# Performance work log

Hardware: AMD Instinct MI355X
Metric: run time of the kernel (lower is better)

## Reference

```python
import jax, jax.numpy as jnp
import numpy as np

T, B, D = 1024, 8, 1024
H, DH, FF = 16, 64, 4096
BG = 0.1  # GRU gating bias constant
SCALE = 1.0 / DH ** 0.5


def layer_norm(x, g, b, eps=1e-5):
    mu = jnp.mean(x, axis=-1, keepdims=True)
    var = jnp.var(x, axis=-1, keepdims=True)
    return (x - mu) * jax.lax.rsqrt(var + eps) * g + b


def gru_gate(x, y, W, U, bz):
    # W, U: [3, D, D] stacking (r, z, g) projections; bz: Uz bias
    r = jax.nn.sigmoid(y @ W[0] + x @ U[0])
    z = jax.nn.sigmoid(y @ W[1] + x @ U[1] + bz - BG)
    h = jnp.tanh(y @ W[2] + r * (x @ U[2]))
    return (1.0 - z) * x + z * h


def setup_inputs() -> dict:
    key = jax.random.key(0)
    ks = jax.random.split(key, 16)
    s = 0.02
    inp = {
        "x": jax.random.normal(ks[0], (T, B, D), jnp.float32),
        "Wq": jax.random.normal(ks[1], (D, H * DH), jnp.float32) * s,
        "Wk": jax.random.normal(ks[2], (D, H * DH), jnp.float32) * s,
        "Wv": jax.random.normal(ks[3], (D, H * DH), jnp.float32) * s,
        "Wo": jax.random.normal(ks[4], (H * DH, D), jnp.float32) * s,
        "ln1_g": jnp.ones((D,), jnp.float32),
        "ln1_b": jnp.zeros((D,), jnp.float32),
        "W1": jax.random.normal(ks[5], (D, FF), jnp.float32) * s,
        "b1": jnp.zeros((FF,), jnp.float32),
        "W2": jax.random.normal(ks[6], (FF, D), jnp.float32) * s,
        "b2": jnp.zeros((D,), jnp.float32),
        "ln2_g": jnp.ones((D,), jnp.float32),
        "ln2_b": jnp.zeros((D,), jnp.float32),
        "gate1_W": jax.random.normal(ks[7], (3, D, D), jnp.float32) * s,
        "gate1_U": jax.random.normal(ks[8], (3, D, D), jnp.float32) * s,
        "gate1_bz": jnp.zeros((D,), jnp.float32),
        "gate2_W": jax.random.normal(ks[9], (3, D, D), jnp.float32) * s,
        "gate2_U": jax.random.normal(ks[10], (3, D, D), jnp.float32) * s,
        "gate2_bz": jnp.zeros((D,), jnp.float32),
        "attn_mask": jnp.triu(jnp.ones((T, T), bool), k=1),  # causal: mask j > i
    }
    return inp


def reference(x, Wq, Wk, Wv, Wo, ln1_g, ln1_b, W1, b1, W2, b2,
              ln2_g, ln2_b, gate1_W, gate1_U, gate1_bz,
              gate2_W, gate2_U, gate2_bz, attn_mask):
    # --- multihead attention (pre_lnorm=True) ---
    xn = layer_norm(x, ln1_g, ln1_b)                     # [T,B,D]
    q = (xn @ Wq).reshape(T, B, H, DH)
    k = (xn @ Wk).reshape(T, B, H, DH)
    v = (xn @ Wv).reshape(T, B, H, DH)
    scores = jnp.einsum('ibhd,jbhd->ijbh', q, k) * SCALE  # [T,T,B,H]
    scores = jnp.where(attn_mask[:, :, None, None], -jnp.inf, scores)
    probs = jax.nn.softmax(scores, axis=1)
    attn = jnp.einsum('ijbh,jbhd->ibhd', probs, v).reshape(T, B, H * DH)
    src2 = attn @ Wo                                      # [T,B,D]
    # --- GRU gate 1 ---
    src = gru_gate(x, src2, gate1_W, gate1_U, gate1_bz)
    # --- positionwise FFN (pre_lnorm=True) ---
    sn = layer_norm(src, ln2_g, ln2_b)
    ff = jax.nn.relu(sn @ W1 + b1) @ W2 + b2
    # --- GRU gate 2 ---
    return gru_gate(src, ff, gate2_W, gate2_U, gate2_bz)
```

## Files before the change

kernel.cpp:

```cpp
#include <hip/hip_runtime.h>
#include <hip/hip_bf16.h>

#define T_  1024
#define B_  8
#define D_  1024
#define H_  16
#define DH_ 64
#define FF_ 4096
#define MROWS (T_*B_)

typedef __attribute__((ext_vector_type(8))) short short8;
typedef __attribute__((ext_vector_type(4))) float f32x4;
typedef __attribute__((ext_vector_type(4))) unsigned short us4;
typedef __attribute__((ext_vector_type(4))) unsigned int  u32x4;

__device__ __forceinline__ unsigned short f2b(float f){
  unsigned int u = __builtin_bit_cast(unsigned int, f);
  u += 0x7FFFu + ((u >> 16) & 1u);
  return (unsigned short)(u >> 16);
}
__device__ __forceinline__ float b2f(unsigned short h){
  unsigned int u = ((unsigned int)h) << 16;
  return __builtin_bit_cast(float, u);
}

__device__ __forceinline__ void glds16(const unsigned short* g, unsigned short* l){
  __builtin_amdgcn_global_load_lds(
    (const __attribute__((address_space(1))) unsigned int*)g,
    (__attribute__((address_space(3))) unsigned int*)l, 16, 0, 0);
}

enum { FRELU=1 };

__global__ __launch_bounds__(512, 2) void gemm256(
    const unsigned short* __restrict__ A1, const unsigned short* __restrict__ A2,
    int K1, long lda,
    const unsigned short* __restrict__ Bt, long ldb,
    unsigned short* __restrict__ C, long ldc,
    const float* __restrict__ bias, int K, int flags)
{
  constexpr int BM = 256, BK = 32;
  extern __shared__ char L[];

  int t = threadIdx.x, w = t >> 6, l = t & 63;

  int nx = gridDim.x;
  int nwg = nx * gridDim.y;
  int lin = blockIdx.y*nx + blockIdx.x;
  if (!(nwg & 7)) lin = (lin & 7)*(nwg >> 3) + (lin >> 3);
  int bx = lin % nx, by = lin / nx;
  int m0 = by*BM, n0 = bx*BM;

  int srow[2], sce[2];
  #pragma unroll
  for (int q=0;q<2;q++){
    int p  = q*8192 + w*1024 + l*16;
    int sp = p ^ (((p>>6)&3)<<4);
    srow[q] = sp >> 6;
    sce[q]  = (sp & 63) >> 1;
  }

  auto stage = [&](int buf, int kt){
    int k0 = kt*BK;
    const unsigned short* ap; int ko;
    if (k0 < K1){ ap = A1; ko = k0; } else { ap = A2; ko = k0 - K1; }
    char* ab = L + buf*32768;
    char* bb = ab + 16384;
    #pragma unroll
    for (int q=0;q<2;q++)
      glds16(ap + (long)(m0 + srow[q])*lda + ko + sce[q],
             (unsigned short*)(ab + q*8192 + w*1024));
    #pragma unroll
    for (int q=0;q<2;q++)
      glds16(Bt + (long)(n0 + srow[q])*ldb + k0 + sce[q],
             (unsigned short*)(bb + q*8192 + w*1024));
  };

  f32x4 acc[8][4];
  #pragma unroll
  for (int m=0;m<8;m++)
    #pragma unroll
    for (int n=0;n<4;n++) acc[m][n] = (f32x4){0.f,0.f,0.f,0.f};

  int wr = w >> 2, wc = w & 3;
  int fr = l & 15, fq = l >> 4;
  int nk = K / BK;

  stage(0, 0);
  stage(1, 1);
  asm volatile("s_waitcnt vmcnt(4)" ::: "memory");
  __builtin_amdgcn_s_barrier();
  asm volatile("" ::: "memory");

  int cur = 0;
  for (int kt = 0; kt < nk; ++kt){
    int nxt = cur + 2; if (nxt >= 3) nxt -= 3;
    if (kt + 2 < nk) stage(nxt, kt + 2);

    const char* ab = L + cur*32768;
    const char* bb = ab + 16384;
    short8 af[8], bf[4];
    #pragma unroll
    for (int n=0;n<4;n++){
      int r = wc*64 + n*16 + fr;
      bf[n] = *(const short8*)(bb + ((r*64 + fq*16) ^ ((r&3)<<4)));
    }
    #pragma unroll
    for (int m=0;m<8;m++){
      int r = wr*128 + m*16 + fr;
      af[m] = *(const short8*)(ab + ((r*64 + fq*16) ^ ((r&3)<<4)));
    }
    __builtin_amdgcn_s_setprio(1);
    #pragma unroll
    for (int m=0;m<8;m++)
      #pragma unroll
      for (int n=0;n<4;n++)
        acc[m][n] = __builtin_amdgcn_mfma_f32_16x16x32_bf16(af[m], bf[n], acc[m][n], 0,0,0);
    __builtin_amdgcn_s_setprio(0);

    if (kt + 2 < nk) asm volatile("s_waitcnt vmcnt(4)" ::: "memory");
    else             asm volatile("s_waitcnt vmcnt(0)" ::: "memory");
    __builtin_amdgcn_s_barrier();
    asm volatile("" ::: "memory");
    cur += 1; if (cur >= 3) cur -= 3;
  }

  int r0 = m0 + wr*128 + (fq << 2);
  int c0 = n0 + wc*64 + fr;
  #pragma unroll
  for (int m=0;m<8;m++)
    #pragma unroll
    for (int n=0;n<4;n++){
      int col = c0 + n*16;
      float bv = bias ? bias[col] : 0.f;
      #pragma unroll
      for (int j=0;j<4;j++){
        float v = acc[m][n][j] + bv;
        if (flags & FRELU) v = v > 0.f ? v : 0.f;
        C[(long)(r0 + m*16 + j)*ldc + col] = f2b(v);
      }
    }
}

__global__ __launch_bounds__(256) void gemm_bf16(
    const unsigned short* __restrict__ A1, const unsigned short* __restrict__ A2,
    int K1, long lda,
    const unsigned short* __restrict__ Bt, long ldb,
    unsigned short* __restrict__ C, long ldc,
    const float* __restrict__ bias, int K, int flags)
{
  constexpr int BM = 128, BK = 32;
  __shared__ unsigned short As[2][BM*BK];
  __shared__ unsigned short Bs[2][BM*BK];

  int t = threadIdx.x, w = t >> 6, l = t & 63;

  int nx = gridDim.x;
  int nwg = nx * gridDim.y;
  int lin = blockIdx.y*nx + blockIdx.x;
  if (!(nwg & 7)) lin = (lin & 7)*(nwg >> 3) + (lin >> 3);
  int bx = lin % nx, by = lin / nx;
  int m0 = by*BM, n0 = bx*BM;

  int arow = t >> 2, acol = (t & 3) * 8;
  const unsigned short* a1p = A1 + (long)(m0 + arow)*lda + acol;
  const unsigned short* a2p = A2 + (long)(m0 + arow)*lda + acol - K1;
  const unsigned short* bp  = Bt + (long)(n0 + arow)*ldb + acol;

  auto stage = [&](int buf, int k0){
    const unsigned short* ap = (k0 < K1) ? a1p : a2p;
    glds16(ap + k0,          &As[buf][      w*512]);
    glds16(ap + 64*lda + k0, &As[buf][2048 + w*512]);
    glds16(bp + k0,          &Bs[buf][      w*512]);
    glds16(bp + 64*ldb + k0, &Bs[buf][2048 + w*512]);
  };

  f32x4 acc[4][4];
  #pragma unroll
  for (int m=0;m<4;m++)
    #pragma unroll
    for (int n=0;n<4;n++) acc[m][n] = (f32x4){0.f,0.f,0.f,0.f};

  int wm = (w >> 1) * 64, wn = (w & 1) * 64;
  int fr = l & 15, fk = (l >> 4) * 8;
  int nk = K / BK;

  stage(0, 0);
  __syncthreads();

  for (int kt = 0; kt < nk; ++kt){
    int cur = kt & 1;
    if (kt + 1 < nk) stage(cur ^ 1, (kt+1)*BK);

    short8 af[4], bf[4];
    #pragma unroll
    for (int m=0;m<4;m++) af[m] = *(const short8*)&As[cur][(wm + m*16 + fr)*BK + fk];
    #pragma unroll
    for (int n=0;n<4;n++) bf[n] = *(const short8*)&Bs[cur][(wn + n*16 + fr)*BK + fk];
    #pragma unroll
    for (int m=0;m<4;m++)
      #pragma unroll
      for (int n=0;n<4;n++)
        acc[m][n] = __builtin_amdgcn_mfma_f32_16x16x32_bf16(af[m], bf[n], acc[m][n], 0, 0, 0);

    __syncthreads();
  }

  int r0 = m0 + wm + ((l >> 4) << 2);
  int c0 = n0 + wn + fr;
  #pragma unroll
  for (int m=0;m<4;m++)
    #pragma unroll
    for (int n=0;n<4;n++){
      int col = c0 + n*16;
      float bv = bias ? bias[col] : 0.f;
      #pragma unroll
      for (int j=0;j<4;j++){
        float v = acc[m][n][j] + bv;
        if (flags & FRELU) v = v > 0.f ? v : 0.f;
        C[(long)(r0 + m*16 + j)*ldc + col] = f2b(v);
      }
    }
}

__global__ __launch_bounds__(256) void flash_attn(
  const unsigned short* __restrict__ qkv, const unsigned short* __restrict__ vT,
  unsigned short* __restrict__ O)
{
  int p = blockIdx.x, z = blockIdx.y;
  int b = z >> 4, h = z & 15;
  const unsigned short* Vz = vT + (long)z*DH_*T_;

  __shared__ unsigned short Ks[64*64];
  __shared__ unsigned short Vs[64*64];
  __shared__ unsigned short Ps[4][32][72];

  int t = threadIdx.x, w = t >> 6, l = t & 63;
  int fr = l & 15, fg = l >> 4;
  int srow = t >> 2, sc = (t & 3) * 16;

  for (int rep = 0; rep < 2; ++rep){
    int qt = rep ? (7 - p) : p;
    int q0 = qt*128 + w*32;

    short8 qf[2][2];
    #pragma unroll
    for (int m=0;m<2;m++)
      #pragma unroll
      for (int ks=0;ks<2;ks++)
        qf[m][ks] = *(const short8*)(qkv + ((long)(q0 + m*16 + fr)*B_ + b)*3072 + h*DH_ + ks*32 + fg*8);

    f32x4 oacc[2][4];
    float mr[2][4], lr[2][4];
    #pragma unroll
    for (int m=0;m<2;m++){
      #pragma unroll
      for (int n=0;n<4;n++) oacc[m][n] = (f32x4){0.f,0.f,0.f,0.f};
      #pragma unroll
      for (int j=0;j<4;j++){ mr[m][j] = -1e30f; lr[m][j] = 0.f; }
    }

    int nkv = (qt + 1) * 2;
    for (int kt = 0; kt < nkv; ++kt){
      int kv0 = kt * 64;
      __syncthreads();
      {
        const unsigned short* kg = qkv + ((long)(kv0+srow)*B_ + b)*3072 + 1024 + h*DH_ + sc;
        const unsigned short* vg = Vz + (long)srow*T_ + kv0 + sc;
        int rb = srow*128, sw = (srow & 7) << 4;
        *(u32x4*)((char*)Ks + ((rb + sc*2     ) ^ sw)) = *(const u32x4*)(kg);
        *(u32x4*)((char*)Ks + ((rb + sc*2 + 16) ^ sw)) = *(const u32x4*)(kg + 8);
        *(u32x4*)((char*)Vs + ((rb + sc*2     ) ^ sw)) = *(const u32x4*)(vg);
        *(u32x4*)((char*)Vs + ((rb + sc*2 + 16) ^ sw)) = *(const u32x4*)(vg + 8);
      }
      __syncthreads();

      if (kv0 <= q0 + 31){
        f32x4 sacc[2][4];
        #pragma unroll
        for (int m=0;m<2;m++)
          #pragma unroll
          for (int n=0;n<4;n++) sacc[m][n] = (f32x4){0.f,0.f,0.f,0.f};
        __builtin_amdgcn_s_setprio(1);
        #pragma unroll
        for (int ks=0;ks<2;ks++){
          short8 kf[4];
          #pragma unroll
          for (int n=0;n<4;n++){
            int r = n*16 + fr;
            kf[n] = *(const short8*)((const char*)Ks + ((r*128 + ks*64 + fg*16) ^ ((r & 7) << 4)));
          }
          #pragma unroll
          for (int m=0;m<2;m++)
            #pragma unroll
            for (int n=0;n<4;n++)
              sacc[m][n] = __builtin_amdgcn_mfma_f32_16x16x32_bf16(qf[m][ks], kf[n], sacc[m][n], 0,0,0);
        }
        __builtin_amdgcn_s_setprio(0);

        #pragma unroll
        for (int m=0;m<2;m++)
          #pragma unroll
          for (int j=0;j<4;j++){
            int qg = q0 + m*16 + fg*4 + j;
            float vmax = -1e30f;
            #pragma unroll
            for (int n=0;n<4;n++){
              int kg = kv0 + n*16 + fr;
              float s = (kg <= qg) ? sacc[m][n][j]*0.125f : -1e30f;
              sacc[m][n][j] = s;
              vmax = fmaxf(vmax, s);
            }
            #pragma unroll
            for (int msk=1; msk<16; msk<<=1) vmax = fmaxf(vmax, __shfl_xor(vmax, msk));
            float mnew = fmaxf(mr[m][j], vmax);
            float sc_o = __expf(mr[m][j] - mnew);
            mr[m][j] = mnew;
            float rsum = 0.f;
            #pragma unroll
            for (int n=0;n<4;n++){
              float pv = __expf(sacc[m][n][j] - mnew);
              sacc[m][n][j] = pv;
              rsum += pv;
            }
            #pragma unroll
            for (int msk=1; msk<16; msk<<=1) rsum += __shfl_xor(rsum, msk);
            lr[m][j] = lr[m][j]*sc_o + rsum;
            #pragma unroll
            for (int n=0;n<4;n++) oacc[m][n][j] *= sc_o;
          }

        #pragma unroll
        for (int m=0;m<2;m++)
          #pragma unroll
          for (int n=0;n<4;n++)
            #pragma unroll
            for (int j=0;j<4;j++)
              Ps[w][m*16 + fg*4 + j][n*16 + fr] = f2b(sacc[m][n][j]);

        __builtin_amdgcn_s_setprio(1);
        #pragma unroll
        for (int ks=0;ks<2;ks++){
          short8 pf[2], vf[4];
          #pragma unroll
          for (int m=0;m<2;m++) pf[m] = *(const short8*)&Ps[w][m*16+fr][ks*32+fg*8];
          #pragma unroll
          for (int n=0;n<4;n++){
            int r = n*16 + fr;
            vf[n] = *(const short8*)((const char*)Vs + ((r*128 + ks*64 + fg*16) ^ ((r & 7) << 4)));
          }
          #pragma unroll
          for (int m=0;m<2;m++)
            #pragma unroll
            for (int n=0;n<4;n++)
              oacc[m][n] = __builtin_amdgcn_mfma_f32_16x16x32_bf16(pf[m], vf[n], oacc[m][n], 0,0,0);
        }
        __builtin_amdgcn_s_setprio(0);
      }
    }

    #pragma unroll
    for (int m=0;m<2;m++)
      #pragma unroll
      for (int j=0;j<4;j++){
        float inv = 1.f / lr[m][j];
        long i = q0 + m*16 + fg*4 + j;
        #pragma unroll
        for (int n=0;n<4;n++)
          O[(i*B_ + b)*(long)D_ + h*DH_ + n*16 + fr] = f2b(oacc[m][n][j] * inv);
      }
  }
}

__global__ __launch_bounds__(256) void ln_bf16(const float* __restrict__ X,
    const float* __restrict__ g, const float* __restrict__ bta,
    unsigned short* __restrict__ out)
{
  long row = blockIdx.x;
  int t = threadIdx.x;
  f32x4 xv = ((const f32x4*)(X + row*D_))[t];
  float s = xv[0]+xv[1]+xv[2]+xv[3];
  float q = xv[0]*xv[0]+xv[1]*xv[1]+xv[2]*xv[2]+xv[3]*xv[3];
  #pragma unroll
  for (int o=32;o;o>>=1){ s += __shfl_xor(s,o); q += __shfl_xor(q,o); }
  __shared__ float rs[4], rq[4];
  int w = t >> 6;
  if ((t & 63) == 0){ rs[w]=s; rq[w]=q; }
  __syncthreads();
  s = rs[0]+rs[1]+rs[2]+rs[3];
  q = rq[0]+rq[1]+rq[2]+rq[3];
  float mean = s * (1.f/D_);
  float var  = q * (1.f/D_) - mean*mean;
  float rstd = rsqrtf(var + 1e-5f);
  f32x4 gv = ((const f32x4*)g)[t];
  f32x4 bv = ((const f32x4*)bta)[t];
  us4 o;
  #pragma unroll
  for (int jj=0;jj<4;jj++) o[jj] = f2b((xv[jj]-mean)*rstd*gv[jj] + bv[jj]);
  ((us4*)(out + row*D_))[t] = o;
}

__global__ __launch_bounds__(256) void tr_f2b(const float* __restrict__ src,
    unsigned short* __restrict__ dst, int N, long ldd)
{
  __shared__ float tile[32][33];
  int k0 = blockIdx.x*32, n0 = blockIdx.y*32;
  int tx = threadIdx.x & 31, ty = threadIdx.x >> 5;
  #pragma unroll
  for (int i=0;i<4;i++)
    tile[ty+i*8][tx] = src[(long)(k0+ty+i*8)*N + n0 + tx];
  __syncthreads();
  #pragma unroll
  for (int i=0;i<4;i++)
    dst[(long)(n0+ty+i*8)*ldd + k0 + tx] = f2b(tile[tx][ty+i*8]);
}

__global__ __launch_bounds__(256) void build_vT(const unsigned short* __restrict__ vsrc,
                                                unsigned short* __restrict__ vT)
{
  __shared__ unsigned short tile[32][33];
  int z = blockIdx.z, b = z >> 4, h = z & 15;
  int t0 = blockIdx.x*32, d0 = blockIdx.y*32;
  int tx = threadIdx.x & 31, ty = threadIdx.x >> 5;
  #pragma unroll
  for (int i=0;i<4;i++)
    tile[ty+i*8][tx] = vsrc[((long)(t0+ty+i*8)*B_ + b)*3072 + h*DH_ + d0 + tx];
  __syncthreads();
  #pragma unroll
  for (int i=0;i<4;i++)
    vT[(long)z*DH_*T_ + (long)(d0+ty+i*8)*T_ + t0 + tx] = tile[tx][ty+i*8];
}

__global__ __launch_bounds__(256) void cast_f2b(const float* __restrict__ src,
                                                unsigned short* __restrict__ dst)
{
  long i = ((long)blockIdx.x*256 + threadIdx.x)*4;
  f32x4 v = *(const f32x4*)(src + i);
  us4 o;
  #pragma unroll
  for (int jj=0;jj<4;jj++) o[jj] = f2b(v[jj]);
  *(us4*)(dst + i) = o;
}

__global__ __launch_bounds__(256) void gru_combine(
  const unsigned short* __restrict__ rz,
  const unsigned short* __restrict__ ya, const unsigned short* __restrict__ xb,
  const float* __restrict__ xin, const float* __restrict__ bz,
  float* __restrict__ of, unsigned short* __restrict__ ob)
{
  long i = ((long)blockIdx.x*256 + threadIdx.x)*4;
  long row = i >> 10; int col = (int)(i & 1023);
  us4 r4 = *(const us4*)(rz + row*2048 + col);
  us4 z4 = *(const us4*)(rz + row*2048 + 1024 + col);
  us4 a4 = *(const us4*)(ya + i);
  us4 b4 = *(const us4*)(xb + i);
  f32x4 xv = *(const f32x4*)(xin + i);
  f32x4 bzv = *(const f32x4*)(bz + col);
  f32x4 o;
  #pragma unroll
  for (int jj=0;jj<4;jj++){
    float r = 1.f/(1.f + __expf(-b2f(r4[jj])));
    float z = 1.f/(1.f + __expf(-(b2f(z4[jj]) + bzv[jj] - 0.1f)));
    float h = tanhf(b2f(a4[jj]) + r*b2f(b4[jj]));
    o[jj] = (1.f - z)*xv[jj] + z*h;
  }
  *(f32x4*)(of+i) = o;
  if (ob){
    us4 q;
    #pragma unroll
    for (int jj=0;jj<4;jj++) q[jj] = f2b(o[jj]);
    *(us4*)(ob+i) = q;
  }
}

extern "C" void kernel_launch(void* const* d_in, const int* in_sizes, int n_in,
                              void* d_out, int out_size, void* d_ws, size_t ws_size,
                              hipStream_t stream)
{
  const float* x    = (const float*)d_in[0];
  const float* Wq   = (const float*)d_in[1];
  const float* Wk   = (const float*)d_in[2];
  const float* Wv   = (const float*)d_in[3];
  const float* Wo   = (const float*)d_in[4];
  const float* ln1g = (const float*)d_in[5];
  const float* ln1b = (const float*)d_in[6];
  const float* W1   = (const float*)d_in[7];
  const float* b1   = (const float*)d_in[8];
  const float* W2   = (const float*)d_in[9];
  const float* b2   = (const float*)d_in[10];
  const float* ln2g = (const float*)d_in[11];
  const float* ln2b = (const float*)d_in[12];
  const float* g1W  = (const float*)d_in[13];
  const float* g1U  = (const float*)d_in[14];
  const float* g1bz = (const float*)d_in[15];
  const float* g2W  = (const float*)d_in[16];
  const float* g2U  = (const float*)d_in[17];
  const float* g2bz = (const float*)d_in[18];
  float* out = (float*)d_out;

  const size_t MB = 1u << 20;
  if (ws_size < 144*MB) return;
  char* base = (char*)d_ws;

  (void)hipFuncSetAttribute((const void*)gemm256,
                            hipFuncAttributeMaxDynamicSharedMemorySize, 98304);

  unsigned short* W    = (unsigned short*)(base);
  unsigned short* x_bf = (unsigned short*)(base + 16*MB);
  unsigned short* sbf  = (unsigned short*)(base + 32*MB);
  unsigned short* src2 = (unsigned short*)(base + 48*MB);
  unsigned short* qkv  = (unsigned short*)(base + 64*MB);
  unsigned short* vT   = (unsigned short*)(base + 112*MB);
  unsigned short* attn = (unsigned short*)(base + 128*MB);
  unsigned short* xn   = attn;
  unsigned short* rz   = (unsigned short*)(base + 64*MB);
  unsigned short* yab  = (unsigned short*)(base + 96*MB);
  unsigned short* xbb  = (unsigned short*)(base + 112*MB);
  unsigned short* sn   = (unsigned short*)(base + 64*MB);
  unsigned short* ff1  = (unsigned short*)(base + 80*MB);
  unsigned short* ffb  = src2;

  const size_t E1M = 1048576;
  unsigned short* BtRZ = W;
  unsigned short* W2g  = W + 4*E1M;
  unsigned short* U2g  = W + 5*E1M;
  unsigned short* W1T  = W;
  unsigned short* W2T  = W + 4*E1M;
  unsigned short* Wqkv = W;
  unsigned short* WoT  = W + 3*E1M;

  dim3 blk(256);
  auto G = [&](const unsigned short* A1, const unsigned short* A2, int K1, long lda,
               const unsigned short* Bt, long ldb, unsigned short* C, long ldc,
               const float* bias, int M, int N, int K, int flags){
    gemm_bf16<<<dim3(N/128, M/128), blk, 0, stream>>>(A1,A2,K1,lda,Bt,ldb,C,ldc,bias,K,flags);
  };
  auto G2 = [&](const unsigned short* A1, const unsigned short* A2, int K1, long lda,
                const unsigned short* Bt, long ldb, unsigned short* C, long ldc,
                const float* bias, int M, int N, int K, int flags){
    gemm256<<<dim3(N/256, M/256), dim3(512), 98304, stream>>>(A1,A2,K1,lda,Bt,ldb,C,ldc,bias,K,flags);
  };

  tr_f2b<<<dim3(32,32), blk, 0, stream>>>(Wq, Wqkv,          D_, D_);
  tr_f2b<<<dim3(32,32), blk, 0, stream>>>(Wk, Wqkv + 1*E1M,  D_, D_);
  tr_f2b<<<dim3(32,32), blk, 0, stream>>>(Wv, Wqkv + 2*E1M,  D_, D_);
  tr_f2b<<<dim3(32,32), blk, 0, stream>>>(Wo, WoT,           D_, D_);
  cast_f2b<<<dim3(MROWS), blk, 0, stream>>>(x, x_bf);

  ln_bf16<<<dim3(MROWS), blk, 0, stream>>>(x, ln1g, ln1b, xn);
  G2(xn, xn, D_, D_, Wqkv, D_, qkv, 3072, nullptr, MROWS, 3072, D_, 0);
  build_vT<<<dim3(32,2,128), blk, 0, stream>>>(qkv + 2048, vT);
  flash_attn<<<dim3(4, B_*H_), blk, 0, stream>>>(qkv, vT, attn);
  G(attn, attn, D_, D_, WoT, D_, src2, D_, nullptr, MROWS, D_, D_, 0);

  tr_f2b<<<dim3(32,32), blk, 0, stream>>>(g1W + 0*E1M, BtRZ,                    D_, 2048);
  tr_f2b<<<dim3(32,32), blk, 0, stream>>>(g1U + 0*E1M, BtRZ + 1024,             D_, 2048);
  tr_f2b<<<dim3(32,32), blk, 0, stream>>>(g1W + 1*E1M, BtRZ + 1024*2048,        D_, 2048);
  tr_f2b<<<dim3(32,32), blk, 0, stream>>>(g1U + 1*E1M, BtRZ + 1024*2048 + 1024, D_, 2048);
  tr_f2b<<<dim3(32,32), blk, 0, stream>>>(g1W + 2*E1M, W2g, D_, D_);
  tr_f2b<<<dim3(32,32), blk, 0, stream>>>(g1U + 2*E1M, U2g, D_, D_);
  G2(src2, x_bf, D_, D_, BtRZ, 2048, rz, 2048, nullptr, MROWS, 2048, 2048, 0);
  G(src2, src2, D_, D_, W2g, D_, yab, D_, nullptr, MROWS, D_, D_, 0);
  G(x_bf, x_bf, D_, D_, U2g, D_, xbb, D_, nullptr, MROWS, D_, D_, 0);
  gru_combine<<<dim3(MROWS), blk, 0, stream>>>(rz, yab, xbb, x, g1bz, out, sbf);

  tr_f2b<<<dim3(32,128), blk, 0, stream>>>(W1, W1T, FF_, D_);
  tr_f2b<<<dim3(128,32), blk, 0, stream>>>(W2, W2T, D_, FF_);
  ln_bf16<<<dim3(MROWS), blk, 0, stream>>>(out, ln2g, ln2b, sn);
  G2(sn, sn, D_, D_, W1T, D_, ff1, FF_, b1, MROWS, FF_, D_, FRELU);
  G(ff1, ff1, FF_, FF_, W2T, FF_, ffb, D_, b2, MROWS, D_, FF_, 0);

  tr_f2b<<<dim3(32,32), blk, 0, stream>>>(g2W + 0*E1M, BtRZ,                    D_, 2048);
  tr_f2b<<<dim3(32,32), blk, 0, stream>>>(g2U + 0*E1M, BtRZ + 1024,             D_, 2048);
  tr_f2b<<<dim3(32,32), blk, 0, stream>>>(g2W + 1*E1M, BtRZ + 1024*2048,        D_, 2048);
  tr_f2b<<<dim3(32,32), blk, 0, stream>>>(g2U + 1*E1M, BtRZ + 1024*2048 + 1024, D_, 2048);
  tr_f2b<<<dim3(32,32), blk, 0, stream>>>(g2W + 2*E1M, W2g, D_, D_);
  tr_f2b<<<dim3(32,32), blk, 0, stream>>>(g2U + 2*E1M, U2g, D_, D_);
  G2(ffb, sbf, D_, D_, BtRZ, 2048, rz, 2048, nullptr, MROWS, 2048, 2048, 0);
  G(ffb, ffb, D_, D_, W2g, D_, yab, D_, nullptr, MROWS, D_, D_, 0);
  G(sbf, sbf, D_, D_, U2g, D_, xbb, D_, nullptr, MROWS, D_, D_, 0);
  gru_combine<<<dim3(MROWS), blk, 0, stream>>>(rz, yab, xbb, out, g2bz, out, nullptr);
}
```

Before: 782.1 us.

## Change LDS swizzles in GEMMs and fuse LN, cast and gate transposes

Changes the LDS XOR swizzle in both bf16 GEMM kernels so it uses row bits 1-2 instead of bits 0-1, and adds a swizzle to the 128-tile GEMM, to reduce shared-memory bank conflicts on fragment reads. Fuses the bf16 cast of x into the first layernorm kernel, fuses the second layernorm into the first GRU combine kernel, and merges six gate-weight transposes into one batched launch per gate. These fusions remove several kernel launches and extra passes over activations. The new swizzles must match exactly between the global-to-LDS staging and the fragment loads, and sn now reuses the x_bf buffer.

New measurement: 749.1 us. -4.2%, faster.

```diff
diff --git a/kernel.cpp b/kernel.cpp
--- a/kernel.cpp
+++ b/kernel.cpp
@@ -55,7 +55,7 @@
   #pragma unroll
   for (int q=0;q<2;q++){
     int p  = q*8192 + w*1024 + l*16;
-    int sp = p ^ (((p>>6)&3)<<4);
+    int sp = p ^ (((p>>7)&3)<<4);
     srow[q] = sp >> 6;
     sce[q]  = (sp & 63) >> 1;
   }
@@ -103,12 +103,12 @@
     #pragma unroll
     for (int n=0;n<4;n++){
       int r = wc*64 + n*16 + fr;
-      bf[n] = *(const short8*)(bb + ((r*64 + fq*16) ^ ((r&3)<<4)));
+      bf[n] = *(const short8*)(bb + ((r*64 + fq*16) ^ (((r>>1)&3)<<4)));
     }
     #pragma unroll
     for (int m=0;m<8;m++){
       int r = wr*128 + m*16 + fr;
-      af[m] = *(const short8*)(ab + ((r*64 + fq*16) ^ ((r&3)<<4)));
+      af[m] = *(const short8*)(ab + ((r*64 + fq*16) ^ (((r>>1)&3)<<4)));
     }
     __builtin_amdgcn_s_setprio(1);
     #pragma unroll
@@ -162,7 +162,8 @@
   int bx = lin % nx, by = lin / nx;
   int m0 = by*BM, n0 = bx*BM;
 
-  int arow = t >> 2, acol = (t & 3) * 8;
+  int arow = t >> 2;
+  int acol = ((t & 3) ^ ((arow >> 1) & 3)) * 8;
   const unsigned short* a1p = A1 + (long)(m0 + arow)*lda + acol;
   const unsigned short* a2p = A2 + (long)(m0 + arow)*lda + acol - K1;
   const unsigned short* bp  = Bt + (long)(n0 + arow)*ldb + acol;
@@ -194,9 +195,15 @@
 
     short8 af[4], bf[4];
     #pragma unroll
-    for (int m=0;m<4;m++) af[m] = *(const short8*)&As[cur][(wm + m*16 + fr)*BK + fk];
-    #pragma unroll
-    for (int n=0;n<4;n++) bf[n] = *(const short8*)&Bs[cur][(wn + n*16 + fr)*BK + fk];
+    for (int m=0;m<4;m++){
+      int rr = wm + m*16 + fr;
+      af[m] = *(const short8*)&As[cur][rr*BK + (fk ^ ((((rr)>>1)&3)<<3))];
+    }
+    #pragma unroll
+    for (int n=0;n<4;n++){
+      int rr = wn + n*16 + fr;
+      bf[n] = *(const short8*)&Bs[cur][rr*BK + (fk ^ ((((rr)>>1)&3)<<3))];
+    }
     #pragma unroll
     for (int m=0;m<4;m++)
       #pragma unroll
@@ -372,9 +379,9 @@
   }
 }
 
-__global__ __launch_bounds__(256) void ln_bf16(const float* __restrict__ X,
+__global__ __launch_bounds__(256) void ln_cast(const float* __restrict__ X,
     const float* __restrict__ g, const float* __restrict__ bta,
-    unsigned short* __restrict__ out)
+    unsigned short* __restrict__ xn, unsigned short* __restrict__ xbf)
 {
   long row = blockIdx.x;
   int t = threadIdx.x;
@@ -394,10 +401,14 @@
   float rstd = rsqrtf(var + 1e-5f);
   f32x4 gv = ((const f32x4*)g)[t];
   f32x4 bv = ((const f32x4*)bta)[t];
-  us4 o;
-  #pragma unroll
-  for (int jj=0;jj<4;jj++) o[jj] = f2b((xv[jj]-mean)*rstd*gv[jj] + bv[jj]);
-  ((us4*)(out + row*D_))[t] = o;
+  us4 o, raw;
+  #pragma unroll
+  for (int jj=0;jj<4;jj++){
+    o[jj]   = f2b((xv[jj]-mean)*rstd*gv[jj] + bv[jj]);
+    raw[jj] = f2b(xv[jj]);
+  }
+  ((us4*)(xn  + row*D_))[t] = o;
+  ((us4*)(xbf + row*D_))[t] = raw;
 }
 
 __global__ __launch_bounds__(256) void tr_f2b(const float* __restrict__ src,
@@ -409,6 +420,27 @@
   #pragma unroll
   for (int i=0;i<4;i++)
     tile[ty+i*8][tx] = src[(long)(k0+ty+i*8)*N + n0 + tx];
+  __syncthreads();
+  #pragma unroll
+  for (int i=0;i<4;i++)
+    dst[(long)(n0+ty+i*8)*ldd + k0 + tx] = f2b(tile[tx][ty+i*8]);
+}
+
+__global__ __launch_bounds__(256) void tr_gate(const float* __restrict__ gW,
+    const float* __restrict__ gU, unsigned short* __restrict__ Wb)
+{
+  __shared__ float tile[32][33];
+  int z = blockIdx.z;
+  int c = z >> 1;
+  const float* src = ((z & 1) ? gU : gW) + (size_t)c*1048576;
+  unsigned short* dst; long ldd;
+  if (c < 2){ dst = Wb + (size_t)c*(1024*2048) + (z&1)*1024; ldd = 2048; }
+  else      { dst = Wb + (size_t)(4 + (z&1))*1048576;        ldd = 1024; }
+  int k0 = blockIdx.x*32, n0 = blockIdx.y*32;
+  int tx = threadIdx.x & 31, ty = threadIdx.x >> 5;
+  #pragma unroll
+  for (int i=0;i<4;i++)
+    tile[ty+i*8][tx] = src[(long)(k0+ty+i*8)*1024 + n0 + tx];
   __syncthreads();
   #pragma unroll
   for (int i=0;i<4;i++)
@@ -431,25 +463,18 @@
     vT[(long)z*DH_*T_ + (long)(d0+ty+i*8)*T_ + t0 + tx] = tile[tx][ty+i*8];
 }
 
-__global__ __launch_bounds__(256) void cast_f2b(const float* __restrict__ src,
-                                                unsigned short* __restrict__ dst)
-{
-  long i = ((long)blockIdx.x*256 + threadIdx.x)*4;
-  f32x4 v = *(const f32x4*)(src + i);
-  us4 o;
-  #pragma unroll
-  for (int jj=0;jj<4;jj++) o[jj] = f2b(v[jj]);
-  *(us4*)(dst + i) = o;
-}
-
 __global__ __launch_bounds__(256) void gru_combine(
   const unsigned short* __restrict__ rz,
   const unsigned short* __restrict__ ya, const unsigned short* __restrict__ xb,
   const float* __restrict__ xin, const float* __restrict__ bz,
-  float* __restrict__ of, unsigned short* __restrict__ ob)
-{
-  long i = ((long)blockIdx.x*256 + threadIdx.x)*4;
-  long row = i >> 10; int col = (int)(i & 1023);
+  float* __restrict__ of, unsigned short* __restrict__ ob,
+  const float* __restrict__ lng, const float* __restrict__ lnb,
+  unsigned short* __restrict__ sn)
+{
+  int t = threadIdx.x;
+  long row = blockIdx.x;
+  long i = row*1024 + t*4;
+  int col = t*4;
   us4 r4 = *(const us4*)(rz + row*2048 + col);
   us4 z4 = *(const us4*)(rz + row*2048 + 1024 + col);
   us4 a4 = *(const us4*)(ya + i);
@@ -470,6 +495,27 @@
     #pragma unroll
     for (int jj=0;jj<4;jj++) q[jj] = f2b(o[jj]);
     *(us4*)(ob+i) = q;
+  }
+  if (sn){
+    float s = o[0]+o[1]+o[2]+o[3];
+    float q = o[0]*o[0]+o[1]*o[1]+o[2]*o[2]+o[3]*o[3];
+    #pragma unroll
+    for (int off=32;off;off>>=1){ s += __shfl_xor(s,off); q += __shfl_xor(q,off); }
+    __shared__ float rs[4], rq[4];
+    int w = t >> 6;
+    if ((t & 63) == 0){ rs[w]=s; rq[w]=q; }
+    __syncthreads();
+    s = rs[0]+rs[1]+rs[2]+rs[3];
+    q = rq[0]+rq[1]+rq[2]+rq[3];
+    float mean = s * (1.f/D_);
+    float var  = q * (1.f/D_) - mean*mean;
+    float rstd = rsqrtf(var + 1e-5f);
+    f32x4 gv = ((const f32x4*)lng)[t];
+    f32x4 bv = ((const f32x4*)lnb)[t];
+    us4 oq;
+    #pragma unroll
+    for (int jj=0;jj<4;jj++) oq[jj] = f2b((o[jj]-mean)*rstd*gv[jj] + bv[jj]);
+    *(us4*)(sn+i) = oq;
   }
 }
 
@@ -516,7 +562,7 @@
   unsigned short* rz   = (unsigned short*)(base + 64*MB);
   unsigned short* yab  = (unsigned short*)(base + 96*MB);
   unsigned short* xbb  = (unsigned short*)(base + 112*MB);
-  unsigned short* sn   = (unsigned short*)(base + 64*MB);
+  unsigned short* sn   = x_bf;
   unsigned short* ff1  = (unsigned short*)(base + 80*MB);
   unsigned short* ffb  = src2;
 
@@ -545,39 +591,27 @@
   tr_f2b<<<dim3(32,32), blk, 0, stream>>>(Wk, Wqkv + 1*E1M,  D_, D_);
   tr_f2b<<<dim3(32,32), blk, 0, stream>>>(Wv, Wqkv + 2*E1M,  D_, D_);
   tr_f2b<<<dim3(32,32), blk, 0, stream>>>(Wo, WoT,           D_, D_);
-  cast_f2b<<<dim3(MROWS), blk, 0, stream>>>(x, x_bf);
-
-  ln_bf16<<<dim3(MROWS), blk, 0, stream>>>(x, ln1g, ln1b, xn);
+  ln_cast<<<dim3(MROWS), blk, 0, stream>>>(x, ln1g, ln1b, xn, x_bf);
+
   G2(xn, xn, D_, D_, Wqkv, D_, qkv, 3072, nullptr, MROWS, 3072, D_, 0);
   build_vT<<<dim3(32,2,128), blk, 0, stream>>>(qkv + 2048, vT);
   flash_attn<<<dim3(4, B_*H_), blk, 0, stream>>>(qkv, vT, attn);
   G(attn, attn, D_, D_, WoT, D_, src2, D_, nullptr, MROWS, D_, D_, 0);
 
-  tr_f2b<<<dim3(32,32), blk, 0, stream>>>(g1W + 0*E1M, BtRZ,                    D_, 2048);
-  tr_f2b<<<dim3(32,32), blk, 0, stream>>>(g1U + 0*E1M, BtRZ + 1024,             D_, 2048);
-  tr_f2b<<<dim3(32,32), blk, 0, stream>>>(g1W + 1*E1M, BtRZ + 1024*2048,        D_, 2048);
-  tr_f2b<<<dim3(32,32), blk, 0, stream>>>(g1U + 1*E1M, BtRZ + 1024*2048 + 1024, D_, 2048);
-  tr_f2b<<<dim3(32,32), blk, 0, stream>>>(g1W + 2*E1M, W2g, D_, D_);
-  tr_f2b<<<dim3(32,32), blk, 0, stream>>>(g1U + 2*E1M, U2g, D_, D_);
+  tr_gate<<<dim3(32,32,6), blk, 0, stream>>>(g1W, g1U, W);
   G2(src2, x_bf, D_, D_, BtRZ, 2048, rz, 2048, nullptr, MROWS, 2048, 2048, 0);
   G(src2, src2, D_, D_, W2g, D_, yab, D_, nullptr, MROWS, D_, D_, 0);
   G(x_bf, x_bf, D_, D_, U2g, D_, xbb, D_, nullptr, MROWS, D_, D_, 0);
-  gru_combine<<<dim3(MROWS), blk, 0, stream>>>(rz, yab, xbb, x, g1bz, out, sbf);
+  gru_combine<<<dim3(MROWS), blk, 0, stream>>>(rz, yab, xbb, x, g1bz, out, sbf, ln2g, ln2b, sn);
 
   tr_f2b<<<dim3(32,128), blk, 0, stream>>>(W1, W1T, FF_, D_);
   tr_f2b<<<dim3(128,32), blk, 0, stream>>>(W2, W2T, D_, FF_);
-  ln_bf16<<<dim3(MROWS), blk, 0, stream>>>(out, ln2g, ln2b, sn);
   G2(sn, sn, D_, D_, W1T, D_, ff1, FF_, b1, MROWS, FF_, D_, FRELU);
   G(ff1, ff1, FF_, FF_, W2T, FF_, ffb, D_, b2, MROWS, D_, FF_, 0);
 
-  tr_f2b<<<dim3(32,32), blk, 0, stream>>>(g2W + 0*E1M, BtRZ,                    D_, 2048);
-  tr_f2b<<<dim3(32,32), blk, 0, stream>>>(g2U + 0*E1M, BtRZ + 1024,             D_, 2048);
-  tr_f2b<<<dim3(32,32), blk, 0, stream>>>(g2W + 1*E1M, BtRZ + 1024*2048,        D_, 2048);
-  tr_f2b<<<dim3(32,32), blk, 0, stream>>>(g2U + 1*E1M, BtRZ + 1024*2048 + 1024, D_, 2048);
-  tr_f2b<<<dim3(32,32), blk, 0, stream>>>(g2W + 2*E1M, W2g, D_, D_);
-  tr_f2b<<<dim3(32,32), blk, 0, stream>>>(g2U + 2*E1M, U2g, D_, D_);
+  tr_gate<<<dim3(32,32,6), blk, 0, stream>>>(g2W, g2U, W);
   G2(ffb, sbf, D_, D_, BtRZ, 2048, rz, 2048, nullptr, MROWS, 2048, 2048, 0);
   G(ffb, ffb, D_, D_, W2g, D_, yab, D_, nullptr, MROWS, D_, D_, 0);
   G(sbf, sbf, D_, D_, U2g, D_, xbb, D_, nullptr, MROWS, D_, D_, 0);
-  gru_combine<<<dim3(MROWS), blk, 0, stream>>>(rz, yab, xbb, out, g2bz, out, nullptr);
-}
+  gru_combine<<<dim3(MROWS), blk, 0, stream>>>(rz, yab, xbb, out, g2bz, out, nullptr, nullptr, nullptr, nullptr);
+}
```
